# Performance work log

Hardware: AMD Instinct MI355X
Metric: run time of the kernel (lower is better)

## Reference

```python
import jax, jax.numpy as jnp
import numpy as np

D_MODEL = 1024
N_HEADS = 16
DH = D_MODEL // N_HEADS            # 64
Q_PROJ = D_MODEL // 2              # 512
KV_PROJ = 2 * D_MODEL // 3         # 682
LN_EPS = 1e-5                      # torch.nn.LayerNorm default


def _layernorm(x, gamma, beta, eps=LN_EPS):
    mu = jnp.mean(x, axis=-1, keepdims=True)
    var = jnp.mean(jnp.square(x - mu), axis=-1, keepdims=True)
    return (x - mu) * jax.lax.rsqrt(var + eps) * gamma + beta


def setup_inputs() -> dict:
    key = jax.random.key(0)
    ks = jax.random.split(key, 6)
    B, L = 2, 2048
    x = jax.random.normal(ks[0], (B, L, D_MODEL), dtype=jnp.float32)
    W_dq = 0.01 * jax.random.normal(ks[1], (D_MODEL, Q_PROJ), dtype=jnp.float32)
    W_uq = 0.01 * jax.random.normal(ks[2], (Q_PROJ, D_MODEL), dtype=jnp.float32)
    W_dkv = 0.01 * jax.random.normal(ks[3], (D_MODEL, KV_PROJ), dtype=jnp.float32)
    W_ukv = 0.01 * jax.random.normal(ks[4], (KV_PROJ, 2 * D_MODEL), dtype=jnp.float32)
    q_gamma = jnp.ones((Q_PROJ,), jnp.float32)
    q_beta = jnp.zeros((Q_PROJ,), jnp.float32)
    kv_gamma = jnp.ones((KV_PROJ,), jnp.float32)
    kv_beta = jnp.zeros((KV_PROJ,), jnp.float32)
    return {"x": x, "W_dq": W_dq, "W_uq": W_uq, "q_gamma": q_gamma,
            "q_beta": q_beta, "W_dkv": W_dkv, "W_ukv": W_ukv,
            "kv_gamma": kv_gamma, "kv_beta": kv_beta}


def reference(x, W_dq, W_uq, q_gamma, q_beta, W_dkv, W_ukv, kv_gamma, kv_beta):
    B, L, _ = x.shape
    # low-rank Q path: down-project, layernorm, up-project
    compressed_q = _layernorm(x @ W_dq, q_gamma, q_beta)      # [B,L,Q_PROJ]
    Q = compressed_q @ W_uq                                    # [B,L,D]
    # low-rank joint KV path
    compressed_kv = _layernorm(x @ W_dkv, kv_gamma, kv_beta)  # [B,L,KV_PROJ]
    KV = compressed_kv @ W_ukv                                 # [B,L,2D]
    K, V = KV[..., :D_MODEL], KV[..., D_MODEL:]
    # split heads: [B,H,L,dh]
    q = Q.reshape(B, L, N_HEADS, DH).transpose(0, 2, 1, 3)
    k = K.reshape(B, L, N_HEADS, DH).transpose(0, 2, 1, 3)
    v = V.reshape(B, L, N_HEADS, DH).transpose(0, 2, 1, 3)
    scores = jnp.einsum('bhqd,bhkd->bhqk', q, k) / jnp.sqrt(jnp.float32(DH))
    attn = jax.nn.softmax(scores, axis=-1)                     # [B,H,L,L]
    # NOTE: original forward computes feat = LN(dropout(fc(attn@v)) + x) but
    # discards it, returning (x, attn, compressed_kv). Dead code omitted.
    return (x, attn, compressed_kv)
```

## Files before the change

### kernel.cpp

```cpp
#include <hip/hip_runtime.h>

typedef __bf16 bf16;
typedef __bf16 bf16x4 __attribute__((ext_vector_type(4)));
typedef __bf16 bf16x8 __attribute__((ext_vector_type(8)));
typedef float f32x4 __attribute__((ext_vector_type(4)));

#define GCAST(p) ((const __attribute__((address_space(1))) void*)(p))
#define LCAST(p) ((__attribute__((address_space(3))) void*)(p))

#define ML 4096
#define DM 1024
#define QP 512
#define KVP 682
#define KVPP 768
#define NDOWN 1280

__device__ __forceinline__ void trans_tile(const float* __restrict__ src, int srcLD,
                                           int K, int N, int NP,
                                           bf16* __restrict__ dst, int dstLD, int dn,
                                           int bx, int by, float (*tile)[65]) {
    const int k0 = bx * 64, n0 = by * 64;
    const int c = threadIdx.x & 63, r4 = threadIdx.x >> 6;
    #pragma unroll
    for (int rr = r4; rr < 64; rr += 4) {
        int k = k0 + rr, n = n0 + c;
        tile[rr][c] = (k < K && n < N) ? src[(size_t)k * srcLD + n] : 0.f;
    }
    __syncthreads();
    #pragma unroll
    for (int nn = r4; nn < 64; nn += 4) {
        int n = n0 + nn, k = k0 + c;
        if (n < NP && k < dstLD)
            dst[(size_t)(n + dn) * dstLD + k] = (bf16)tile[c][nn];
    }
}

__global__ __launch_bounds__(256) void prep(const f32x4* __restrict__ x4,
                                            f32x4* __restrict__ out0,
                                            bf16* __restrict__ xb,
                                            const float* __restrict__ Wdq,
                                            const float* __restrict__ Wdkv,
                                            const float* __restrict__ Wuq,
                                            const float* __restrict__ Wukv,
                                            bf16* __restrict__ Wdt,
                                            bf16* __restrict__ Wuqt,
                                            bf16* __restrict__ Wukvt) {
    __shared__ float tile[64][65];
    int bid = blockIdx.x;
    if (bid < 4096) {
        int i = bid * 256 + threadIdx.x;
        f32x4 v = x4[i];
        __builtin_nontemporal_store(v, &out0[i]);
        bf16x4 b;
        b[0] = (bf16)v.x; b[1] = (bf16)v.y; b[2] = (bf16)v.z; b[3] = (bf16)v.w;
        *(bf16x4*)(xb + (size_t)i * 4) = b;
        return;
    }
    int rel = bid - 4096;
    if (rel < 128) {
        trans_tile(Wdq, QP, DM, QP, QP, Wdt, DM, 0, rel & 15, rel >> 4, tile);
    } else if (rel < 320) {
        rel -= 128;
        trans_tile(Wdkv, KVP, DM, KVP, KVPP, Wdt, DM, QP, rel & 15, rel >> 4, tile);
    } else if (rel < 448) {
        rel -= 320;
        trans_tile(Wuq, DM, QP, DM, DM, Wuqt, QP, 0, rel & 7, rel >> 3, tile);
    } else {
        rel -= 448;
        trans_tile(Wukv, 2048, KVP, DM, DM, Wukvt, KVPP, 0, rel % 12, rel / 12, tile);
    }
}

__device__ __forceinline__ void gemm_body(const bf16* __restrict__ A,
                                          const bf16* __restrict__ Bt,
                                          bf16* __restrict__ C,
                                          int N, int K, int bx, int by,
                                          bf16* As, bf16* Bs) {
    const int t = threadIdx.x;
    const int w = t >> 6, lane = t & 63;
    const int bm = bx * 128, bn = by * 128;
    const int wr = (w >> 1) * 64, wc = (w & 1) * 64;
    const int r16 = lane & 15, g4 = lane >> 4;
    const int srow = w * 16 + (lane >> 2);
    const int scol = (lane & 3) * 8;

    f32x4 acc[4][4] = {};

    for (int k0 = 0; k0 < K; k0 += 32) {
        #pragma unroll
        for (int r = 0; r < 2; ++r) {
            const bf16* ga = A + (size_t)(bm + r*64 + srow) * K + k0 + scol;
            __builtin_amdgcn_global_load_lds(GCAST(ga), LCAST(&As[r*2048 + w*512]), 16, 0, 0);
            const bf16* gb = Bt + (size_t)(bn + r*64 + srow) * K + k0 + scol;
            __builtin_amdgcn_global_load_lds(GCAST(gb), LCAST(&Bs[r*2048 + w*512]), 16, 0, 0);
        }
        __syncthreads();
        bf16x8 af[4], bfr[4];
        #pragma unroll
        for (int i = 0; i < 4; ++i)
            af[i] = *(const bf16x8*)&As[(wr + i*16 + r16) * 32 + g4*8];
        #pragma unroll
        for (int j = 0; j < 4; ++j)
            bfr[j] = *(const bf16x8*)&Bs[(wc + j*16 + r16) * 32 + g4*8];
        #pragma unroll
        for (int i = 0; i < 4; ++i)
            #pragma unroll
            for (int j = 0; j < 4; ++j)
                acc[i][j] = __builtin_amdgcn_mfma_f32_16x16x32_bf16(af[i], bfr[j], acc[i][j], 0, 0, 0);
        __syncthreads();
    }
    #pragma unroll
    for (int i = 0; i < 4; ++i)
        #pragma unroll
        for (int j = 0; j < 4; ++j)
            #pragma unroll
            for (int r = 0; r < 4; ++r) {
                int row = bm + wr + i*16 + g4*4 + r;
                int col = bn + wc + j*16 + r16;
                C[(size_t)row * N + col] = (bf16)acc[i][j][r];
            }
}

__global__ __launch_bounds__(256) void gemm_down(const bf16* __restrict__ A,
                                                 const bf16* __restrict__ Bt,
                                                 bf16* __restrict__ C) {
    __shared__ bf16 As[128 * 32];
    __shared__ bf16 Bs[128 * 32];
    gemm_body(A, Bt, C, NDOWN, DM, blockIdx.x, blockIdx.y, As, Bs);
}

__global__ __launch_bounds__(256) void gemm_up2(const bf16* __restrict__ Cq,
                                                const bf16* __restrict__ Wuqt,
                                                bf16* __restrict__ Qb,
                                                const bf16* __restrict__ Ckv,
                                                const bf16* __restrict__ Wukvt,
                                                bf16* __restrict__ Kb) {
    __shared__ bf16 As[128 * 32];
    __shared__ bf16 Bs[128 * 32];
    if (blockIdx.z == 0)
        gemm_body(Cq,  Wuqt,  Qb, DM, QP,   blockIdx.x, blockIdx.y, As, Bs);
    else
        gemm_body(Ckv, Wukvt, Kb, DM, KVPP, blockIdx.x, blockIdx.y, As, Bs);
}

__global__ __launch_bounds__(256) void ln_wave(const bf16* __restrict__ Cdown,
                                               const float* __restrict__ qg,
                                               const float* __restrict__ qb,
                                               const float* __restrict__ kvg,
                                               const float* __restrict__ kvb,
                                               bf16* __restrict__ Cq,
                                               float* __restrict__ out2,
                                               bf16* __restrict__ Ckv) {
    const int w = threadIdx.x >> 6, lane = threadIdx.x & 63;
    const int row = blockIdx.x * 4 + w;
    const bf16* src = Cdown + (size_t)row * NDOWN;

    {
        bf16x8 v = *(const bf16x8*)(src + lane * 8);
        float f[8], s = 0.f, sq = 0.f;
        #pragma unroll
        for (int i = 0; i < 8; ++i) {
            f[i] = (float)v[i]; s += f[i]; sq += f[i] * f[i];
        }
        #pragma unroll
        for (int m = 1; m < 64; m <<= 1) {
            s += __shfl_xor(s, m); sq += __shfl_xor(sq, m);
        }
        float mu = s * (1.f / 512.f);
        float rs = rsqrtf(sq * (1.f / 512.f) - mu * mu + 1e-5f);
        bf16x8 o;
        #pragma unroll
        for (int i = 0; i < 8; ++i)
            o[i] = (bf16)((f[i] - mu) * rs * qg[lane * 8 + i] + qb[lane * 8 + i]);
        *(bf16x8*)(Cq + (size_t)row * QP + lane * 8) = o;
    }
    {
        const bf16* skv = src + QP;
        float f[11], s = 0.f, sq = 0.f;
        #pragma unroll
        for (int i = 0; i < 11; ++i) {
            int j = lane + i * 64;
            f[i] = (j < KVP) ? (float)skv[j] : 0.f;
            s += f[i]; sq += f[i] * f[i];
        }
        #pragma unroll
        for (int m = 1; m < 64; m <<= 1) {
            s += __shfl_xor(s, m); sq += __shfl_xor(sq, m);
        }
        float mu = s * (1.f / 682.f);
        float rs = rsqrtf(sq * (1.f / 682.f) - mu * mu + 1e-5f);
        #pragma unroll
        for (int i = 0; i < 11; ++i) {
            int j = lane + i * 64;
            if (j < KVP) {
                float y = (f[i] - mu) * rs * kvg[j] + kvb[j];
                __builtin_nontemporal_store(y, &out2[(size_t)row * KVP + j]);
                Ckv[(size_t)row * KVPP + j] = (bf16)y;
            } else if (j < KVPP) {
                Ckv[(size_t)row * KVPP + j] = (bf16)0.f;
            }
        }
    }
}

__global__ __launch_bounds__(512, 2) void attn_k(const bf16* __restrict__ Qb,
                                                 const bf16* __restrict__ Kb,
                                                 float* __restrict__ out1) {
    __shared__ bf16 Qs[16 * 64];
    __shared__ float reds[8][16];
    __shared__ bf16 P[16 * 2048];

    const int t = threadIdx.x, w = t >> 6, lane = t & 63;
    const int flat = blockIdx.x;
    const int xcd = flat & 7, local = flat >> 3;
    const int qblk = local & 127;
    const int bh = (xcd << 2) | (local >> 7);
    const int b = bh >> 4, h = bh & 15;
    const int q0 = qblk * 16;

    for (int i = t; i < 1024; i += 512) {
        int qr = i >> 6, d = i & 63;
        Qs[i] = Qb[(size_t)(b*2048 + q0 + qr) * DM + h*64 + d];
    }
    __syncthreads();

    const int r16 = lane & 15, g4 = lane >> 4;
    bf16x8 qf0 = *(const bf16x8*)&Qs[r16*64 + g4*8];
    bf16x8 qf1 = *(const bf16x8*)&Qs[r16*64 + 32 + g4*8];

    const bf16* kbase = Kb + (size_t)b * 2048 * DM + h*64;
    const int colw = w * 256;

    float sm = 0.f;
    #pragma unroll
    for (int ni = 0; ni < 16; ++ni) {
        const bf16* kr = kbase + (size_t)(colw + ni*16 + r16) * DM + g4*8;
        bf16x8 k0 = *(const bf16x8*)kr;
        bf16x8 k1 = *(const bf16x8*)(kr + 32);
        f32x4 c = {};
        c = __builtin_amdgcn_mfma_f32_16x16x32_bf16(k0, qf0, c, 0, 0, 0);
        c = __builtin_amdgcn_mfma_f32_16x16x32_bf16(k1, qf1, c, 0, 0, 0);
        bf16x4 pv;
        #pragma unroll
        for (int r = 0; r < 4; ++r) {
            float e = __expf(c[r] * 0.125f);
            sm += e;
            pv[r] = (bf16)e;
        }
        int byte = (r16*4096 + colw*2 + ni*32 + g4*8) ^ ((r16 & 7) << 4);
        *(bf16x4*)((char*)P + byte) = pv;
    }
    sm += __shfl_xor(sm, 16);
    sm += __shfl_xor(sm, 32);
    if (g4 == 0) reds[w][r16] = sm;
    __syncthreads();

    #pragma unroll
    for (int rr = 0; rr < 2; ++rr) {
        int row = w * 2 + rr;
        float s = 0.f;
        #pragma unroll
        for (int ww = 0; ww < 8; ++ww) s += reds[ww][row];
        float inv = 1.f / s;
        float* rowout = out1 + ((size_t)(bh * 2048 + q0 + row)) * 2048;
        const char* rowp = (const char*)P + row * 4096;
        const int xr = (row & 7) << 4;
        #pragma unroll
        for (int c = 0; c < 8; ++c) {
            int byte = (c*512 + lane*8) ^ xr;
            bf16x4 pv = *(const bf16x4*)(rowp + byte);
            f32x4 v;
            v[0] = (float)pv[0] * inv;
            v[1] = (float)pv[1] * inv;
            v[2] = (float)pv[2] * inv;
            v[3] = (float)pv[3] * inv;
            __builtin_nontemporal_store(v, (f32x4*)(rowout + c*256 + lane*4));
        }
    }
}

extern "C" void kernel_launch(void* const* d_in, const int* in_sizes, int n_in,
                              void* d_out, int out_size, void* d_ws, size_t ws_size,
                              hipStream_t stream) {
    const float* x    = (const float*)d_in[0];
    const float* Wdq  = (const float*)d_in[1];
    const float* Wuq  = (const float*)d_in[2];
    const float* qg   = (const float*)d_in[3];
    const float* qbt  = (const float*)d_in[4];
    const float* Wdkv = (const float*)d_in[5];
    const float* Wukv = (const float*)d_in[6];
    const float* kvg  = (const float*)d_in[7];
    const float* kvb  = (const float*)d_in[8];

    float* out0 = (float*)d_out;
    float* out1 = out0 + (size_t)4194304;
    float* out2 = out1 + (size_t)134217728;

    char* ws = (char*)d_ws;
    bf16* Xbf   = (bf16*)(ws + 0);
    bf16* Wdt   = (bf16*)(ws + 8388608);
    bf16* Wuqt  = (bf16*)(ws + 11010048);
    bf16* Wukvt = (bf16*)(ws + 12058624);
    bf16* Cdown = (bf16*)(ws + 13631488);
    bf16* Cq    = (bf16*)(ws + 24117248);
    bf16* Ckv   = (bf16*)(ws + 28311552);
    bf16* Qb    = (bf16*)(ws + 34603008);
    bf16* Kb    = (bf16*)(ws + 42991616);

    prep<<<4736, 256, 0, stream>>>((const f32x4*)x, (f32x4*)out0, Xbf,
                                   Wdq, Wdkv, Wuq, Wukv, Wdt, Wuqt, Wukvt);
    gemm_down<<<dim3(ML/128, NDOWN/128), 256, 0, stream>>>(Xbf, Wdt, Cdown);
    ln_wave<<<ML/4, 256, 0, stream>>>(Cdown, qg, qbt, kvg, kvb, Cq, out2, Ckv);
    gemm_up2<<<dim3(ML/128, DM/128, 2), 256, 0, stream>>>(Cq, Wuqt, Qb, Ckv, Wukvt, Kb);
    attn_k<<<4096, 512, 0, stream>>>(Qb, Kb, out1);
}
```

Measured before the change: 209.0 us.

## Double GEMM K-tile to 64 with XOR-swizzled LDS and trimmed KV K

The shared bf16 GEMM body now stages 64-wide K slices instead of 32, which halves the number of barrier pairs and loop iterations per output tile. An XOR swizzle on the 8-element column groups in LDS is meant to spread fragment reads across banks. The KV up-projection now loops over K=704 rather than the padded 768, skipping zero padding, and separate leading dimensions are added so this works. In exchange LDS use per block doubles, which can lower occupancy, and the change only touches the GEMMs, not the attention and softmax stages.

```diff
diff --git a/kernel.cpp b/kernel.cpp
--- a/kernel.cpp
+++ b/kernel.cpp
@@ -74,39 +74,47 @@
 __device__ __forceinline__ void gemm_body(const bf16* __restrict__ A,
                                           const bf16* __restrict__ Bt,
                                           bf16* __restrict__ C,
-                                          int N, int K, int bx, int by,
+                                          int N, int K, int lda, int ldb,
+                                          int bx, int by,
                                           bf16* As, bf16* Bs) {
     const int t = threadIdx.x;
     const int w = t >> 6, lane = t & 63;
     const int bm = bx * 128, bn = by * 128;
     const int wr = (w >> 1) * 64, wc = (w & 1) * 64;
     const int r16 = lane & 15, g4 = lane >> 4;
-    const int srow = w * 16 + (lane >> 2);
-    const int scol = (lane & 3) * 8;
+
+    const int srow8 = lane >> 3;
+    const int scg   = (lane & 7) ^ (srow8 & 3);
 
     f32x4 acc[4][4] = {};
 
-    for (int k0 = 0; k0 < K; k0 += 32) {
-        #pragma unroll
-        for (int r = 0; r < 2; ++r) {
-            const bf16* ga = A + (size_t)(bm + r*64 + srow) * K + k0 + scol;
-            __builtin_amdgcn_global_load_lds(GCAST(ga), LCAST(&As[r*2048 + w*512]), 16, 0, 0);
-            const bf16* gb = Bt + (size_t)(bn + r*64 + srow) * K + k0 + scol;
-            __builtin_amdgcn_global_load_lds(GCAST(gb), LCAST(&Bs[r*2048 + w*512]), 16, 0, 0);
+    const int rsw = r16 & 3;
+
+    for (int k0 = 0; k0 < K; k0 += 64) {
+        #pragma unroll
+        for (int r = 0; r < 4; ++r) {
+            const int chunk = w * 4 + r;
+            const bf16* ga = A + (size_t)(bm + chunk*8 + srow8) * lda + k0 + scg*8;
+            __builtin_amdgcn_global_load_lds(GCAST(ga), LCAST(&As[chunk*512]), 16, 0, 0);
+            const bf16* gb = Bt + (size_t)(bn + chunk*8 + srow8) * ldb + k0 + scg*8;
+            __builtin_amdgcn_global_load_lds(GCAST(gb), LCAST(&Bs[chunk*512]), 16, 0, 0);
         }
         __syncthreads();
-        bf16x8 af[4], bfr[4];
-        #pragma unroll
-        for (int i = 0; i < 4; ++i)
-            af[i] = *(const bf16x8*)&As[(wr + i*16 + r16) * 32 + g4*8];
-        #pragma unroll
-        for (int j = 0; j < 4; ++j)
-            bfr[j] = *(const bf16x8*)&Bs[(wc + j*16 + r16) * 32 + g4*8];
-        #pragma unroll
-        for (int i = 0; i < 4; ++i)
+        #pragma unroll
+        for (int ki = 0; ki < 2; ++ki) {
+            bf16x8 af[4], bfr[4];
+            #pragma unroll
+            for (int i = 0; i < 4; ++i)
+                af[i] = *(const bf16x8*)&As[(wr + i*16 + r16) * 64 + (ki*4 + (g4 ^ rsw)) * 8];
             #pragma unroll
             for (int j = 0; j < 4; ++j)
-                acc[i][j] = __builtin_amdgcn_mfma_f32_16x16x32_bf16(af[i], bfr[j], acc[i][j], 0, 0, 0);
+                bfr[j] = *(const bf16x8*)&Bs[(wc + j*16 + r16) * 64 + (ki*4 + (g4 ^ rsw)) * 8];
+            #pragma unroll
+            for (int i = 0; i < 4; ++i)
+                #pragma unroll
+                for (int j = 0; j < 4; ++j)
+                    acc[i][j] = __builtin_amdgcn_mfma_f32_16x16x32_bf16(af[i], bfr[j], acc[i][j], 0, 0, 0);
+        }
         __syncthreads();
     }
     #pragma unroll
@@ -124,9 +132,9 @@
 __global__ __launch_bounds__(256) void gemm_down(const bf16* __restrict__ A,
                                                  const bf16* __restrict__ Bt,
                                                  bf16* __restrict__ C) {
-    __shared__ bf16 As[128 * 32];
-    __shared__ bf16 Bs[128 * 32];
-    gemm_body(A, Bt, C, NDOWN, DM, blockIdx.x, blockIdx.y, As, Bs);
+    __shared__ bf16 As[128 * 64];
+    __shared__ bf16 Bs[128 * 64];
+    gemm_body(A, Bt, C, NDOWN, DM, DM, DM, blockIdx.x, blockIdx.y, As, Bs);
 }
 
 __global__ __launch_bounds__(256) void gemm_up2(const bf16* __restrict__ Cq,
@@ -135,12 +143,12 @@
                                                 const bf16* __restrict__ Ckv,
                                                 const bf16* __restrict__ Wukvt,
                                                 bf16* __restrict__ Kb) {
-    __shared__ bf16 As[128 * 32];
-    __shared__ bf16 Bs[128 * 32];
+    __shared__ bf16 As[128 * 64];
+    __shared__ bf16 Bs[128 * 64];
     if (blockIdx.z == 0)
-        gemm_body(Cq,  Wuqt,  Qb, DM, QP,   blockIdx.x, blockIdx.y, As, Bs);
+        gemm_body(Cq,  Wuqt,  Qb, DM, QP,  QP,   QP,   blockIdx.x, blockIdx.y, As, Bs);
     else
-        gemm_body(Ckv, Wukvt, Kb, DM, KVPP, blockIdx.x, blockIdx.y, As, Bs);
+        gemm_body(Ckv, Wukvt, Kb, DM, 704, KVPP, KVPP, blockIdx.x, blockIdx.y, As, Bs);
 }
 
 __global__ __launch_bounds__(256) void ln_wave(const bf16* __restrict__ Cdown,
```

Result: faster. 203.6 us (-2.6%).
